# Kernel tuning notes

Hardware: AMD Instinct MI355X
Metric: run time of the kernel (lower is better)

## Reference

```python
import jax, jax.numpy as jnp
import numpy as np

N_CLS = 1000
FEAT_DIM = 1024
BATCH = 32768
PROTO_M = 0.95
TEMP = 0.1
BASE_TEMP = 0.1


def setup_inputs() -> dict:
    key = jax.random.key(0)
    k1, k2, k3 = jax.random.split(key, 3)
    features = jax.random.normal(k1, (BATCH, FEAT_DIM), dtype=jnp.float32)
    labels = jax.random.randint(k2, (BATCH,), 0, N_CLS)
    p = jax.random.normal(k3, (N_CLS, FEAT_DIM), dtype=jnp.float32)
    prototypes = p / jnp.maximum(jnp.linalg.norm(p, axis=1, keepdims=True), 1e-12)
    return {"features": features, "prototypes": prototypes, "labels": labels}


def _l2_normalize(x, eps=1e-12):
    # F.normalize(x, dim=0) semantics: x / max(||x||_2, eps)
    return x / jnp.maximum(jnp.linalg.norm(x), eps)


def _ema_update(prototypes, features, labels):
    # Sequential per-sample EMA + renormalize (faithful to the torch for-loop:
    # later samples with the same label see earlier updates).
    def step(protos, fl):
        f, l = fl
        row = _l2_normalize(protos[l] * PROTO_M + f * (1.0 - PROTO_M))
        return protos.at[l].set(row), None

    prototypes, _ = jax.lax.scan(step, prototypes, (features, labels))
    return prototypes


def reference(features, prototypes, labels):
    protos = _ema_update(prototypes, features, labels)  # [n_cls, feat]
    logits = jnp.matmul(protos, protos.T) / TEMP        # [n_cls, n_cls]
    # mask = (1 - eye) * logits_mask, where logits_mask also zeros the diagonal
    mask = 1.0 - jnp.eye(N_CLS, dtype=logits.dtype)
    mean_prob_neg = jnp.log((mask * jnp.exp(logits)).sum(axis=1) / mask.sum(axis=1))
    # torch drops NaNs; with n_cls > 1 every row has n_cls-1 negatives, so none occur
    loss = (TEMP / BASE_TEMP) * jnp.mean(mean_prob_neg)
    return loss
```

## Files before the change

### kernel.cpp

```cpp
#include <hip/hip_runtime.h>
#include <hip/hip_bf16.h>
#include <math.h>

#define N_CLS 1000
#define FEAT  1024
#define BATCH 32768
#define NBLK_H 128
#define CHUNK  256
#define LPITCH 72
#define GRAM_BLOCKS 256

typedef short short8 __attribute__((ext_vector_type(8)));
typedef float f32x4  __attribute__((ext_vector_type(4)));

__device__ __forceinline__ unsigned short f2bf(float x) {
    union { __hip_bfloat16 h; unsigned short u; } cv;
    cv.h = __float2bfloat16(x);
    return cv.u;
}
__device__ __forceinline__ float bf2f(unsigned short u) {
    union { __hip_bfloat16 h; unsigned short u; } cv;
    cv.u = u;
    return __bfloat162float(cv.h);
}

__global__ __launch_bounds__(256) void hist_kernel(const int* __restrict__ labels,
                                                   unsigned* __restrict__ hist,
                                                   float* __restrict__ S,
                                                   unsigned* __restrict__ counter) {
    __shared__ unsigned cnt[N_CLS];
    const int t = threadIdx.x, b = blockIdx.x;
    if (b == 0) {
        for (int i = t; i < N_CLS; i += 256) S[i] = 0.0f;
        if (t == 0) *counter = 0u;
    }
    for (int i = t; i < N_CLS; i += 256) cnt[i] = 0;
    __syncthreads();
    atomicAdd(&cnt[labels[b * CHUNK + t]], 1u);
    __syncthreads();
    for (int i = t; i < N_CLS; i += 256) hist[(size_t)i * NBLK_H + b] = cnt[i];
}

__global__ __launch_bounds__(256) void scan1_kernel(unsigned* __restrict__ hist,
                                                    unsigned* __restrict__ total) {
    const int l    = blockIdx.x * 4 + (threadIdx.x >> 6);
    const int lane = threadIdx.x & 63;
    unsigned v0 = hist[(size_t)l * NBLK_H + lane];
    unsigned v1 = hist[(size_t)l * NBLK_H + 64 + lane];
    unsigned x0 = v0, x1 = v1;
    #pragma unroll
    for (int off = 1; off < 64; off <<= 1) {
        unsigned u0 = __shfl_up(x0, off, 64);
        if (lane >= off) x0 += u0;
        unsigned u1 = __shfl_up(x1, off, 64);
        if (lane >= off) x1 += u1;
    }
    x1 += __shfl(x0, 63, 64);
    hist[(size_t)l * NBLK_H + lane]      = x0 - v0;
    hist[(size_t)l * NBLK_H + 64 + lane] = x1 - v1;
    if (lane == 63) total[l] = x1;
}

__global__ __launch_bounds__(1024) void scan2_kernel(const unsigned* __restrict__ total,
                                                     unsigned* __restrict__ base) {
    const int t = threadIdx.x;
    unsigned v = (t < N_CLS) ? total[t] : 0u;
    __shared__ unsigned sc[1024];
    sc[t] = v;
    __syncthreads();
    for (int off = 1; off < 1024; off <<= 1) {
        unsigned u = (t >= off) ? sc[t - off] : 0u;
        __syncthreads();
        sc[t] += u;
        __syncthreads();
    }
    if (t < N_CLS) base[t] = sc[t] - v;
}

__global__ __launch_bounds__(256) void scatter_kernel(const int* __restrict__ labels,
                                                      const unsigned* __restrict__ hist,
                                                      const unsigned* __restrict__ base,
                                                      int* __restrict__ sorted_idx) {
    __shared__ int lbl[CHUNK];
    __shared__ unsigned c[N_CLS];
    const int t = threadIdx.x, b = blockIdx.x;
    for (int i = t; i < N_CLS; i += 256) c[i] = 0;
    __syncthreads();
    const int i = b * CHUNK + t;
    const int l = labels[i];
    lbl[t] = l;
    atomicAdd(&c[l], 1u);
    __syncthreads();
    int rank = 0;
    if (c[l] > 1) {
        for (int j = 0; j < t; ++j) rank += (lbl[j] == l);
    }
    sorted_idx[base[l] + hist[(size_t)l * NBLK_H + b] + (unsigned)rank] = i;
}

__device__ __forceinline__ float4 ema4(float4 p, float4 f) {
    p.x = fmaf(0.95f, p.x, 0.05f * f.x);
    p.y = fmaf(0.95f, p.y, 0.05f * f.y);
    p.z = fmaf(0.95f, p.z, 0.05f * f.z);
    p.w = fmaf(0.95f, p.w, 0.05f * f.w);
    return p;
}
__device__ __forceinline__ float dot4(float4 a) {
    return a.x * a.x + a.y * a.y + a.z * a.z + a.w * a.w;
}
__device__ __forceinline__ float4 scale4(float4 a, float s) {
    a.x *= s; a.y *= s; a.z *= s; a.w *= s; return a;
}

__device__ __forceinline__ void ema_step(float4& p0, float4& p1, float4& p2, float4& p3,
                                         float4& x0, float4& x1, float4& x2, float4& x3,
                                         const float* __restrict__ features, int iN, int lane) {
    p0 = ema4(p0, x0); p1 = ema4(p1, x1); p2 = ema4(p2, x2); p3 = ema4(p3, x3);
    const float4* f = (const float4*)(features + (size_t)iN * FEAT);
    x0 = f[lane]; x1 = f[lane + 64]; x2 = f[lane + 128]; x3 = f[lane + 192];
    float ss = dot4(p0) + dot4(p1) + dot4(p2) + dot4(p3);
    #pragma unroll
    for (int o = 32; o; o >>= 1) ss += __shfl_xor(ss, o, 64);
    const float inv = 1.0f / fmaxf(sqrtf(ss), 1e-12f);
    p0 = scale4(p0, inv); p1 = scale4(p1, inv); p2 = scale4(p2, inv); p3 = scale4(p3, inv);
}

__device__ __forceinline__ void write_hl(unsigned short* __restrict__ H,
                                         unsigned short* __restrict__ L,
                                         size_t off, float4 v) {
    ushort4 hi, lo;
    hi.x = f2bf(v.x); lo.x = f2bf(v.x - bf2f(hi.x));
    hi.y = f2bf(v.y); lo.y = f2bf(v.y - bf2f(hi.y));
    hi.z = f2bf(v.z); lo.z = f2bf(v.z - bf2f(hi.z));
    hi.w = f2bf(v.w); lo.w = f2bf(v.w - bf2f(hi.w));
    *(ushort4*)(H + off) = hi;
    *(ushort4*)(L + off) = lo;
}

__global__ __launch_bounds__(256) void ema_kernel(const float* __restrict__ features,
                                                  const float* __restrict__ prototypes,
                                                  const int* __restrict__ sorted_idx,
                                                  const unsigned* __restrict__ base,
                                                  const unsigned* __restrict__ total,
                                                  unsigned short* __restrict__ Hg,
                                                  unsigned short* __restrict__ Lg) {
    const int w    = blockIdx.x * 4 + (threadIdx.x >> 6);
    const int lane = threadIdx.x & 63;
    const float4* pr = (const float4*)(prototypes + (size_t)w * FEAT);
    float4 p0 = pr[lane], p1 = pr[lane + 64], p2 = pr[lane + 128], p3 = pr[lane + 192];

    const int cnt = (int)total[w];
    const int bs  = (int)base[w];
    int myidx = (lane < cnt) ? sorted_idx[bs + lane] : 0;

    #define GETIDX(K) (((K) < cnt) ? (((K) < 64) ? __shfl(myidx, (K), 64) : sorted_idx[bs + (K)]) : 0)

    const int iA = GETIDX(0), iB = GETIDX(1), iC = GETIDX(2);
    const float4* fA = (const float4*)(features + (size_t)iA * FEAT);
    float4 a0 = fA[lane], a1 = fA[lane + 64], a2 = fA[lane + 128], a3 = fA[lane + 192];
    const float4* fB = (const float4*)(features + (size_t)iB * FEAT);
    float4 b0 = fB[lane], b1 = fB[lane + 64], b2 = fB[lane + 128], b3 = fB[lane + 192];
    const float4* fC = (const float4*)(features + (size_t)iC * FEAT);
    float4 c0 = fC[lane], c1 = fC[lane + 64], c2 = fC[lane + 128], c3 = fC[lane + 192];

    int k = 0;
    while (k + 3 <= cnt) {
        ema_step(p0,p1,p2,p3, a0,a1,a2,a3, features, GETIDX(k + 3), lane); ++k;
        ema_step(p0,p1,p2,p3, b0,b1,b2,b3, features, GETIDX(k + 3), lane); ++k;
        ema_step(p0,p1,p2,p3, c0,c1,c2,c3, features, GETIDX(k + 3), lane); ++k;
    }
    if (k < cnt) { ema_step(p0,p1,p2,p3, a0,a1,a2,a3, features, 0, lane); ++k; }
    if (k < cnt) { ema_step(p0,p1,p2,p3, b0,b1,b2,b3, features, 0, lane); ++k; }

    const size_t rb = (size_t)w * FEAT;
    write_hl(Hg, Lg, rb +       4 * lane, p0);
    write_hl(Hg, Lg, rb + 256 + 4 * lane, p1);
    write_hl(Hg, Lg, rb + 512 + 4 * lane, p2);
    write_hl(Hg, Lg, rb + 768 + 4 * lane, p3);
    #undef GETIDX
}

__global__ __launch_bounds__(256) void gram_kernel(const unsigned short* __restrict__ Hg,
                                                   const unsigned short* __restrict__ Lg,
                                                   float* __restrict__ S,
                                                   unsigned* __restrict__ counter,
                                                   float* __restrict__ out) {
    __shared__ short Hms[64 * LPITCH];
    __shared__ short Lms[64 * LPITCH];
    __shared__ short Hns[64 * LPITCH];
    __shared__ short Lns[64 * LPITCH];
    const int t = threadIdx.x;
    const int l = t & 63, wid = t >> 6;
    const int wr = wid >> 1, wc = wid & 1;
    const int m0 = blockIdx.y * 64, n0 = blockIdx.x * 64;
    const int lg = l >> 4, lc = l & 15;

    const short* Hp = (const short*)Hg;
    const short* Lp = (const short*)Lg;

    f32x4 acc[2][2] = {};

    const int r0 = t >> 3,           c0 = t & 7;
    const int r1 = (t + 256) >> 3,   c1 = t & 7;

    for (int k0 = 0; k0 < FEAT; k0 += 64) {
        short8 hm0 = *(const short8*)(Hp + (size_t)(m0 + r0) * FEAT + k0 + c0 * 8);
        short8 hm1 = *(const short8*)(Hp + (size_t)(m0 + r1) * FEAT + k0 + c1 * 8);
        short8 lm0 = *(const short8*)(Lp + (size_t)(m0 + r0) * FEAT + k0 + c0 * 8);
        short8 lm1 = *(const short8*)(Lp + (size_t)(m0 + r1) * FEAT + k0 + c1 * 8);
        short8 hn0 = *(const short8*)(Hp + (size_t)(n0 + r0) * FEAT + k0 + c0 * 8);
        short8 hn1 = *(const short8*)(Hp + (size_t)(n0 + r1) * FEAT + k0 + c1 * 8);
        short8 ln0 = *(const short8*)(Lp + (size_t)(n0 + r0) * FEAT + k0 + c0 * 8);
        short8 ln1 = *(const short8*)(Lp + (size_t)(n0 + r1) * FEAT + k0 + c1 * 8);
        __syncthreads();
        *(short8*)(Hms + r0 * LPITCH + c0 * 8) = hm0;
        *(short8*)(Hms + r1 * LPITCH + c1 * 8) = hm1;
        *(short8*)(Lms + r0 * LPITCH + c0 * 8) = lm0;
        *(short8*)(Lms + r1 * LPITCH + c1 * 8) = lm1;
        *(short8*)(Hns + r0 * LPITCH + c0 * 8) = hn0;
        *(short8*)(Hns + r1 * LPITCH + c1 * 8) = hn1;
        *(short8*)(Lns + r0 * LPITCH + c0 * 8) = ln0;
        *(short8*)(Lns + r1 * LPITCH + c1 * 8) = ln1;
        __syncthreads();
        #pragma unroll
        for (int kk = 0; kk < 2; ++kk) {
            short8 ah[2], al[2], bh[2], bl[2];
            #pragma unroll
            for (int mi = 0; mi < 2; ++mi) {
                ah[mi] = *(const short8*)(Hms + (wr * 32 + mi * 16 + lc) * LPITCH + kk * 32 + lg * 8);
                al[mi] = *(const short8*)(Lms + (wr * 32 + mi * 16 + lc) * LPITCH + kk * 32 + lg * 8);
            }
            #pragma unroll
            for (int ni = 0; ni < 2; ++ni) {
                bh[ni] = *(const short8*)(Hns + (wc * 32 + ni * 16 + lc) * LPITCH + kk * 32 + lg * 8);
                bl[ni] = *(const short8*)(Lns + (wc * 32 + ni * 16 + lc) * LPITCH + kk * 32 + lg * 8);
            }
            #pragma unroll
            for (int mi = 0; mi < 2; ++mi)
                #pragma unroll
                for (int ni = 0; ni < 2; ++ni) {
                    acc[mi][ni] = __builtin_amdgcn_mfma_f32_16x16x32_bf16(ah[mi], bh[ni], acc[mi][ni], 0, 0, 0);
                    acc[mi][ni] = __builtin_amdgcn_mfma_f32_16x16x32_bf16(al[mi], bh[ni], acc[mi][ni], 0, 0, 0);
                    acc[mi][ni] = __builtin_amdgcn_mfma_f32_16x16x32_bf16(ah[mi], bl[ni], acc[mi][ni], 0, 0, 0);
                }
        }
    }

    #pragma unroll
    for (int mi = 0; mi < 2; ++mi) {
        #pragma unroll
        for (int j = 0; j < 4; ++j) {
            const int gr = m0 + wr * 32 + mi * 16 + lg * 4 + j;
            float s = 0.f;
            #pragma unroll
            for (int ni = 0; ni < 2; ++ni) {
                const int gc = n0 + wc * 32 + ni * 16 + lc;
                if (gr < N_CLS && gc < N_CLS && gr != gc) s += expf(acc[mi][ni][j] * 10.0f);
            }
            #pragma unroll
            for (int m = 1; m < 16; m <<= 1) s += __shfl_xor(s, m, 64);
            if (lc == 0 && gr < N_CLS) atomicAdd(&S[gr], s);
        }
    }

    __threadfence();
    __shared__ int amlast;
    if (t == 0) {
        unsigned old = __hip_atomic_fetch_add(counter, 1u, __ATOMIC_ACQ_REL, __HIP_MEMORY_SCOPE_AGENT);
        amlast = (old == GRAM_BLOCKS - 1) ? 1 : 0;
    }
    __syncthreads();
    if (amlast) {
        float a = 0.f;
        for (int i = t; i < N_CLS; i += 256) {
            float sv = __hip_atomic_load(&S[i], __ATOMIC_RELAXED, __HIP_MEMORY_SCOPE_AGENT);
            a += logf(sv);
        }
        #pragma unroll
        for (int o = 32; o; o >>= 1) a += __shfl_xor(a, o, 64);
        __shared__ float red[4];
        if (l == 0) red[wid] = a;
        __syncthreads();
        if (t == 0) {
            float tot = red[0] + red[1] + red[2] + red[3];
            out[0] = tot / (float)N_CLS - logf(999.0f);
        }
    }
}

extern "C" void kernel_launch(void* const* d_in, const int* in_sizes, int n_in,
                              void* d_out, int out_size, void* d_ws, size_t ws_size,
                              hipStream_t stream) {
    const float* features   = (const float*)d_in[0];
    const float* prototypes = (const float*)d_in[1];
    const int*   labels     = (const int*)d_in[2];
    float* out = (float*)d_out;

    char* ws = (char*)d_ws;
    unsigned*       hist    = (unsigned*)(ws);
    unsigned*       base    = (unsigned*)(ws + 0x80000);
    unsigned*       total   = (unsigned*)(ws + 0x81000);
    int*            sorted  = (int*)     (ws + 0x82000);
    float*          S       = (float*)   (ws + 0xA4000);
    unsigned*       counter = (unsigned*)(ws + 0xA5000);
    unsigned short* Hg      = (unsigned short*)(ws + 0x100000);
    unsigned short* Lg      = (unsigned short*)(ws + 0x300000);

    hist_kernel   <<<NBLK_H, 256, 0, stream>>>(labels, hist, S, counter);
    scan1_kernel  <<<250, 256, 0, stream>>>(hist, total);
    scan2_kernel  <<<1, 1024, 0, stream>>>(total, base);
    scatter_kernel<<<NBLK_H, 256, 0, stream>>>(labels, hist, base, sorted);
    ema_kernel    <<<250, 256, 0, stream>>>(features, prototypes, sorted, base, total, Hg, Lg);
    gram_kernel   <<<dim3(16, 16), 256, 0, stream>>>(Hg, Lg, S, counter, out);
}
```

Measured before the change: 262.0 us.

## Defer EMA normalization via scaled recurrence, deepen feature prefetch, fuse scan kernels

Rewrites the sequential per-class EMA so the prototype is kept unnormalized. Each step computes c = 0.05*||q|| and applies q = 0.95 q + c x, so normalization happens once at the end, which takes the reciprocal and the scale off the serial dependency chain. Feature prefetch depth goes from 3 to 4 rows in a 5-register-set rotation to hide more load latency. The two scan kernels are merged into one using a last-block-done atomic counter, which removes one launch. The unnormalized magnitudes could in principle drift, but they stay bounded because each step rescales by the current norm.

```diff
diff --git a/kernel.cpp b/kernel.cpp
--- a/kernel.cpp
+++ b/kernel.cpp
@@ -9,6 +9,7 @@
 #define CHUNK  256
 #define LPITCH 72
 #define GRAM_BLOCKS 256
+#define SCAN_BLOCKS 250
 
 typedef short short8 __attribute__((ext_vector_type(8)));
 typedef float f32x4  __attribute__((ext_vector_type(4)));
@@ -32,7 +33,7 @@
     const int t = threadIdx.x, b = blockIdx.x;
     if (b == 0) {
         for (int i = t; i < N_CLS; i += 256) S[i] = 0.0f;
-        if (t == 0) *counter = 0u;
+        if (t == 0) { counter[0] = 0u; counter[1] = 0u; }
     }
     for (int i = t; i < N_CLS; i += 256) cnt[i] = 0;
     __syncthreads();
@@ -41,10 +42,13 @@
     for (int i = t; i < N_CLS; i += 256) hist[(size_t)i * NBLK_H + b] = cnt[i];
 }
 
-__global__ __launch_bounds__(256) void scan1_kernel(unsigned* __restrict__ hist,
-                                                    unsigned* __restrict__ total) {
-    const int l    = blockIdx.x * 4 + (threadIdx.x >> 6);
-    const int lane = threadIdx.x & 63;
+__global__ __launch_bounds__(256) void scan_kernel(unsigned* __restrict__ hist,
+                                                   unsigned* __restrict__ total,
+                                                   unsigned* __restrict__ base,
+                                                   unsigned* __restrict__ counter) {
+    const int t    = threadIdx.x;
+    const int l    = blockIdx.x * 4 + (t >> 6);
+    const int lane = t & 63;
     unsigned v0 = hist[(size_t)l * NBLK_H + lane];
     unsigned v1 = hist[(size_t)l * NBLK_H + 64 + lane];
     unsigned x0 = v0, x1 = v1;
@@ -59,22 +63,41 @@
     hist[(size_t)l * NBLK_H + lane]      = x0 - v0;
     hist[(size_t)l * NBLK_H + 64 + lane] = x1 - v1;
     if (lane == 63) total[l] = x1;
-}
-
-__global__ __launch_bounds__(1024) void scan2_kernel(const unsigned* __restrict__ total,
-                                                     unsigned* __restrict__ base) {
-    const int t = threadIdx.x;
-    unsigned v = (t < N_CLS) ? total[t] : 0u;
-    __shared__ unsigned sc[1024];
-    sc[t] = v;
-    __syncthreads();
-    for (int off = 1; off < 1024; off <<= 1) {
+
+    __syncthreads();
+    __threadfence();
+    __shared__ int amlast;
+    if (t == 0) {
+        unsigned old = __hip_atomic_fetch_add(&counter[1], 1u, __ATOMIC_ACQ_REL, __HIP_MEMORY_SCOPE_AGENT);
+        amlast = (old == SCAN_BLOCKS - 1) ? 1 : 0;
+    }
+    __syncthreads();
+    if (!amlast) return;
+
+    unsigned v[4];
+    unsigned s = 0;
+    #pragma unroll
+    for (int j = 0; j < 4; ++j) {
+        const int i = t * 4 + j;
+        v[j] = (i < N_CLS) ? __hip_atomic_load(&total[i], __ATOMIC_RELAXED, __HIP_MEMORY_SCOPE_AGENT) : 0u;
+        s += v[j];
+    }
+    __shared__ unsigned sc[256];
+    sc[t] = s;
+    __syncthreads();
+    for (int off = 1; off < 256; off <<= 1) {
         unsigned u = (t >= off) ? sc[t - off] : 0u;
         __syncthreads();
         sc[t] += u;
         __syncthreads();
     }
-    if (t < N_CLS) base[t] = sc[t] - v;
+    unsigned acc = sc[t] - s;
+    #pragma unroll
+    for (int j = 0; j < 4; ++j) {
+        const int i = t * 4 + j;
+        if (i < N_CLS) base[i] = acc;
+        acc += v[j];
+    }
 }
 
 __global__ __launch_bounds__(256) void scatter_kernel(const int* __restrict__ labels,
@@ -98,31 +121,31 @@
     sorted_idx[base[l] + hist[(size_t)l * NBLK_H + b] + (unsigned)rank] = i;
 }
 
-__device__ __forceinline__ float4 ema4(float4 p, float4 f) {
-    p.x = fmaf(0.95f, p.x, 0.05f * f.x);
-    p.y = fmaf(0.95f, p.y, 0.05f * f.y);
-    p.z = fmaf(0.95f, p.z, 0.05f * f.z);
-    p.w = fmaf(0.95f, p.w, 0.05f * f.w);
-    return p;
-}
 __device__ __forceinline__ float dot4(float4 a) {
     return a.x * a.x + a.y * a.y + a.z * a.z + a.w * a.w;
 }
 __device__ __forceinline__ float4 scale4(float4 a, float s) {
     a.x *= s; a.y *= s; a.z *= s; a.w *= s; return a;
 }
-
-__device__ __forceinline__ void ema_step(float4& p0, float4& p1, float4& p2, float4& p3,
-                                         float4& x0, float4& x1, float4& x2, float4& x3,
-                                         const float* __restrict__ features, int iN, int lane) {
-    p0 = ema4(p0, x0); p1 = ema4(p1, x1); p2 = ema4(p2, x2); p3 = ema4(p3, x3);
+__device__ __forceinline__ float4 fq4(float4 q, float4 x, float c) {
+    q.x = fmaf(0.95f, q.x, c * x.x);
+    q.y = fmaf(0.95f, q.y, c * x.y);
+    q.z = fmaf(0.95f, q.z, c * x.z);
+    q.w = fmaf(0.95f, q.w, c * x.w);
+    return q;
+}
+
+__device__ __forceinline__ void ema_q_step(float4& q0, float4& q1, float4& q2, float4& q3,
+                                           float4& xc0, float4& xc1, float4& xc2, float4& xc3,
+                                           float4& xl0, float4& xl1, float4& xl2, float4& xl3,
+                                           const float* __restrict__ features, int iN, int lane) {
     const float4* f = (const float4*)(features + (size_t)iN * FEAT);
-    x0 = f[lane]; x1 = f[lane + 64]; x2 = f[lane + 128]; x3 = f[lane + 192];
-    float ss = dot4(p0) + dot4(p1) + dot4(p2) + dot4(p3);
+    xl0 = f[lane]; xl1 = f[lane + 64]; xl2 = f[lane + 128]; xl3 = f[lane + 192];
+    float ss = dot4(q0) + dot4(q1) + dot4(q2) + dot4(q3);
     #pragma unroll
     for (int o = 32; o; o >>= 1) ss += __shfl_xor(ss, o, 64);
-    const float inv = 1.0f / fmaxf(sqrtf(ss), 1e-12f);
-    p0 = scale4(p0, inv); p1 = scale4(p1, inv); p2 = scale4(p2, inv); p3 = scale4(p3, inv);
+    const float c = 0.05f * sqrtf(ss);
+    q0 = fq4(q0, xc0, c); q1 = fq4(q1, xc1, c); q2 = fq4(q2, xc2, c); q3 = fq4(q3, xc3, c);
 }
 
 __device__ __forceinline__ void write_hl(unsigned short* __restrict__ H,
@@ -147,7 +170,7 @@
     const int w    = blockIdx.x * 4 + (threadIdx.x >> 6);
     const int lane = threadIdx.x & 63;
     const float4* pr = (const float4*)(prototypes + (size_t)w * FEAT);
-    float4 p0 = pr[lane], p1 = pr[lane + 64], p2 = pr[lane + 128], p3 = pr[lane + 192];
+    float4 q0 = pr[lane], q1 = pr[lane + 64], q2 = pr[lane + 128], q3 = pr[lane + 192];
 
     const int cnt = (int)total[w];
     const int bs  = (int)base[w];
@@ -155,29 +178,48 @@
 
     #define GETIDX(K) (((K) < cnt) ? (((K) < 64) ? __shfl(myidx, (K), 64) : sorted_idx[bs + (K)]) : 0)
 
-    const int iA = GETIDX(0), iB = GETIDX(1), iC = GETIDX(2);
-    const float4* fA = (const float4*)(features + (size_t)iA * FEAT);
-    float4 a0 = fA[lane], a1 = fA[lane + 64], a2 = fA[lane + 128], a3 = fA[lane + 192];
-    const float4* fB = (const float4*)(features + (size_t)iB * FEAT);
-    float4 b0 = fB[lane], b1 = fB[lane + 64], b2 = fB[lane + 128], b3 = fB[lane + 192];
-    const float4* fC = (const float4*)(features + (size_t)iC * FEAT);
-    float4 c0 = fC[lane], c1 = fC[lane + 64], c2 = fC[lane + 128], c3 = fC[lane + 192];
+    float4 a0, a1, a2, a3, b0, b1, b2, b3, c0, c1, c2, c3, d0, d1, d2, d3, e0, e1, e2, e3;
+    {
+        const float4* f;
+        f = (const float4*)(features + (size_t)GETIDX(0) * FEAT);
+        a0 = f[lane]; a1 = f[lane + 64]; a2 = f[lane + 128]; a3 = f[lane + 192];
+        f = (const float4*)(features + (size_t)GETIDX(1) * FEAT);
+        b0 = f[lane]; b1 = f[lane + 64]; b2 = f[lane + 128]; b3 = f[lane + 192];
+        f = (const float4*)(features + (size_t)GETIDX(2) * FEAT);
+        c0 = f[lane]; c1 = f[lane + 64]; c2 = f[lane + 128]; c3 = f[lane + 192];
+        f = (const float4*)(features + (size_t)GETIDX(3) * FEAT);
+        d0 = f[lane]; d1 = f[lane + 64]; d2 = f[lane + 128]; d3 = f[lane + 192];
+    }
+
+    #define STEP(C0,C1,C2,C3, L0,L1,L2,L3) \
+        ema_q_step(q0,q1,q2,q3, C0,C1,C2,C3, L0,L1,L2,L3, features, GETIDX(k + 4), lane); ++k;
 
     int k = 0;
-    while (k + 3 <= cnt) {
-        ema_step(p0,p1,p2,p3, a0,a1,a2,a3, features, GETIDX(k + 3), lane); ++k;
-        ema_step(p0,p1,p2,p3, b0,b1,b2,b3, features, GETIDX(k + 3), lane); ++k;
-        ema_step(p0,p1,p2,p3, c0,c1,c2,c3, features, GETIDX(k + 3), lane); ++k;
-    }
-    if (k < cnt) { ema_step(p0,p1,p2,p3, a0,a1,a2,a3, features, 0, lane); ++k; }
-    if (k < cnt) { ema_step(p0,p1,p2,p3, b0,b1,b2,b3, features, 0, lane); ++k; }
+    while (k + 5 <= cnt) {
+        STEP(a0,a1,a2,a3, e0,e1,e2,e3)
+        STEP(b0,b1,b2,b3, a0,a1,a2,a3)
+        STEP(c0,c1,c2,c3, b0,b1,b2,b3)
+        STEP(d0,d1,d2,d3, c0,c1,c2,c3)
+        STEP(e0,e1,e2,e3, d0,d1,d2,d3)
+    }
+    if (k < cnt) { STEP(a0,a1,a2,a3, e0,e1,e2,e3) }
+    if (k < cnt) { STEP(b0,b1,b2,b3, a0,a1,a2,a3) }
+    if (k < cnt) { STEP(c0,c1,c2,c3, b0,b1,b2,b3) }
+    if (k < cnt) { STEP(d0,d1,d2,d3, c0,c1,c2,c3) }
+    #undef STEP
+    #undef GETIDX
+
+    float ss = dot4(q0) + dot4(q1) + dot4(q2) + dot4(q3);
+    #pragma unroll
+    for (int o = 32; o; o >>= 1) ss += __shfl_xor(ss, o, 64);
+    const float inv = (cnt > 0) ? (1.0f / fmaxf(sqrtf(ss), 1e-12f)) : 1.0f;
+    q0 = scale4(q0, inv); q1 = scale4(q1, inv); q2 = scale4(q2, inv); q3 = scale4(q3, inv);
 
     const size_t rb = (size_t)w * FEAT;
-    write_hl(Hg, Lg, rb +       4 * lane, p0);
-    write_hl(Hg, Lg, rb + 256 + 4 * lane, p1);
-    write_hl(Hg, Lg, rb + 512 + 4 * lane, p2);
-    write_hl(Hg, Lg, rb + 768 + 4 * lane, p3);
-    #undef GETIDX
+    write_hl(Hg, Lg, rb +       4 * lane, q0);
+    write_hl(Hg, Lg, rb + 256 + 4 * lane, q1);
+    write_hl(Hg, Lg, rb + 512 + 4 * lane, q2);
+    write_hl(Hg, Lg, rb + 768 + 4 * lane, q3);
 }
 
 __global__ __launch_bounds__(256) void gram_kernel(const unsigned short* __restrict__ Hg,
@@ -266,7 +308,7 @@
     __threadfence();
     __shared__ int amlast;
     if (t == 0) {
-        unsigned old = __hip_atomic_fetch_add(counter, 1u, __ATOMIC_ACQ_REL, __HIP_MEMORY_SCOPE_AGENT);
+        unsigned old = __hip_atomic_fetch_add(&counter[0], 1u, __ATOMIC_ACQ_REL, __HIP_MEMORY_SCOPE_AGENT);
         amlast = (old == GRAM_BLOCKS - 1) ? 1 : 0;
     }
     __syncthreads();
@@ -307,9 +349,8 @@
     unsigned short* Lg      = (unsigned short*)(ws + 0x300000);
 
     hist_kernel   <<<NBLK_H, 256, 0, stream>>>(labels, hist, S, counter);
-    scan1_kernel  <<<250, 256, 0, stream>>>(hist, total);
-    scan2_kernel  <<<1, 1024, 0, stream>>>(total, base);
+    scan_kernel   <<<SCAN_BLOCKS, 256, 0, stream>>>(hist, total, base, counter);
     scatter_kernel<<<NBLK_H, 256, 0, stream>>>(labels, hist, base, sorted);
-    ema_kernel    <<<250, 256, 0, stream>>>(features, prototypes, sorted, base, total, Hg, Lg);
+    ema_kernel    <<<SCAN_BLOCKS, 256, 0, stream>>>(features, prototypes, sorted, base, total, Hg, Lg);
     gram_kernel   <<<dim3(16, 16), 256, 0, stream>>>(Hg, Lg, S, counter, out);
 }
```

Result: slower. 277.3 us (+5.8%).
